# Kernel tuning notes

Hardware: AMD Instinct MI355X
Metric: run time of the kernel (lower is better)

## Reference

```python
import jax, jax.numpy as jnp
import numpy as np

# sizes / constants (mirroring the source module's constants)
M, T_SOL, NX, NY = 12, 64, 256, 256
N_TIMES, NOUT = 50, 256
LX, LY_TARGET = 60.0, 75.0
C_CU_TARGET, C_NI_TARGET = 0.001, 0.0001
T_MAX = 200.0
SIGMA, H, DH = 0.25, 4, 8


def setup_inputs() -> dict:
    key = jax.random.key(0)
    ks = jax.random.split(key, 7)
    u = jax.random.uniform(ks[0], (M, 3), dtype=jnp.float32)
    # rows: (Ly in [30,120], c_Cu in [0,0.0029], c_Ni in [0,0.0018])
    params = jnp.stack([30.0 + 90.0 * u[:, 0], 0.0029 * u[:, 1], 0.0018 * u[:, 2]], axis=1)
    c1_src = jax.random.uniform(ks[1], (M, T_SOL, NX, NY), dtype=jnp.float32) * 0.003
    c2_src = jax.random.uniform(ks[2], (M, T_SOL, NX, NY), dtype=jnp.float32) * 0.002
    Wq = jax.random.normal(ks[3], (H * DH, 3), dtype=jnp.float32) * 0.5
    bq = jax.random.normal(ks[4], (H * DH,), dtype=jnp.float32) * 0.1
    Wk = jax.random.normal(ks[5], (H * DH, 3), dtype=jnp.float32) * 0.5
    bk = jax.random.normal(ks[6], (H * DH,), dtype=jnp.float32) * 0.1
    return {"params": params, "c1_src": c1_src, "c2_src": c2_src,
            "Wq": Wq, "bq": bq, "Wk": Wk, "bk": bk}


def _bilinear_resample(xs, ys, vals, xq, yq):
    """RegularGridInterpolator(linear, fill_value=0) on grid (xs[NX], ys[NY]).
    vals: [T, NX, NY]; query is the outer-product grid xq[PX] x yq[PY].
    Separable bilinear -> [T, PX, PY]."""
    ix = jnp.clip(jnp.searchsorted(xs, xq, side='right') - 1, 0, xs.shape[0] - 2)
    tx = (xq - xs[ix]) / (xs[ix + 1] - xs[ix])
    vx = vals[:, ix, :] * (1.0 - tx)[None, :, None] + vals[:, ix + 1, :] * tx[None, :, None]
    iy = jnp.clip(jnp.searchsorted(ys, yq, side='right') - 1, 0, ys.shape[0] - 2)
    ty = (yq - ys[iy]) / (ys[iy + 1] - ys[iy])
    out = vx[:, :, iy] * (1.0 - ty)[None, None, :] + vx[:, :, iy + 1] * ty[None, None, :]
    inb = ((xq >= xs[0]) & (xq <= xs[-1]))[:, None] & ((yq >= ys[0]) & (yq <= ys[-1]))[None, :]
    return jnp.where(inb[None], out, jnp.float32(0.0))


def _forward(params, c1_src, c2_src, Wq, bq, Wk, bk):
    lys, c_cus, c_nis = params[:, 0], params[:, 1], params[:, 2]
    ly_n = (lys - 30.0) / 90.0
    ccu_n = c_cus / 0.0029
    cni_n = c_nis / 0.0018
    p = jnp.stack([ly_n, ccu_n, cni_n], axis=1)                      # [M,3]
    t = jnp.array([[(LY_TARGET - 30.0) / 90.0,
                    C_CU_TARGET / 0.0029,
                    C_NI_TARGET / 0.0018]], dtype=params.dtype)       # [1,3]
    Q = (t @ Wq.T + bq).reshape(1, H, DH)
    K = (p @ Wk.T + bk).reshape(-1, H, DH)
    attn = jnp.einsum('nhd,mhd->nmh', K, Q) / (DH ** 0.5)            # [M,1,H]
    attn_w = jax.nn.softmax(attn, axis=0).mean(axis=2)[:, 0]         # [M]
    dist2 = (((ly_n - t[0, 0]) / SIGMA) ** 2
             + ((ccu_n - t[0, 1]) / SIGMA) ** 2
             + ((cni_n - t[0, 2]) / SIGMA) ** 2)
    sw = jnp.exp(-dist2 / 2.0)
    sw = sw / sw.sum()
    w = attn_w * sw
    w = w / w.sum()                                                  # [M]

    # grids: source x shared; per-solution y grid rescaled to [0, LY_TARGET]
    xs = jnp.linspace(0.0, LX, NX)
    ys_scaled = (jnp.linspace(0.0, 1.0, NY)[None, :] * lys[:, None]) * (LY_TARGET / lys)[:, None]  # [M,NY]
    xq = jnp.linspace(0.0, LX, NOUT)
    yq = jnp.linspace(0.0, LY_TARGET, NOUT)

    times = jnp.linspace(0.0, min(T_MAX, T_MAX), N_TIMES)
    tidx = jnp.clip((times / T_MAX * T_SOL).astype(jnp.int32), 0, T_SOL - 1)  # [T]
    c1_sel = c1_src[:, tidx]                                          # [M,T,NX,NY]
    c2_sel = c2_src[:, tidx]

    res1, res2 = jax.vmap(
        lambda ys, v1, v2: (_bilinear_resample(xs, ys, v1, xq, yq),
                            _bilinear_resample(xs, ys, v2, xq, yq))
    )(ys_scaled, c1_sel, c2_sel)                                      # each [M,T,NOUT,NOUT]

    c1 = jnp.einsum('m,mtij->tij', w, res1)
    c2 = jnp.einsum('m,mtij->tij', w, res2)
    c1 = c1.at[:, :, 0].set(C_CU_TARGET)
    c2 = c2.at[:, :, -1].set(C_NI_TARGET)
    return jnp.stack([c1, c2])                                        # [2,T,NOUT,NOUT]


def reference(params, c1_src, c2_src, Wq, bq, Wk, bk):
    return _forward(params, c1_src, c2_src, Wq, bq, Wk, bk)
```

## Files before the change

kernel.cpp:

```cpp
#include <hip/hip_runtime.h>

#define MM    12
#define TSOL  64
#define NXX   256
#define NYY   256
#define NTT   50
#define NOUTT 256

__device__ float g_wm1[MM * NOUTT];
__device__ float g_wc [MM * NOUTT];
__device__ float g_wp1[MM * NOUTT];

__global__ __launch_bounds__(256) void ai_setup_kernel(
    const float* __restrict__ params,
    const float* __restrict__ Wq, const float* __restrict__ bq,
    const float* __restrict__ Wk, const float* __restrict__ bk)
{
    const int k = threadIdx.x;
    const int m = blockIdx.x;

    __shared__ float s_attn[MM][4];
    __shared__ float s_sw[MM];
    __shared__ float s_wm;
    __shared__ float s_ys[NYY];

    if (k < MM) {
        float ly = params[k * 3 + 0];
        float p0 = (ly - 30.0f) / 90.0f;
        float p1 = params[k * 3 + 1] / 0.0029f;
        float p2 = params[k * 3 + 2] / 0.0018f;
        const float t0 = 0.5f;
        const float t1 = 0.001f / 0.0029f;
        const float t2 = 0.0001f / 0.0018f;
        for (int h = 0; h < 4; ++h) {
            float acc = 0.0f;
            for (int d = 0; d < 8; ++d) {
                int o = h * 8 + d;
                float q  = t0 * Wq[o * 3 + 0] + t1 * Wq[o * 3 + 1] + t2 * Wq[o * 3 + 2] + bq[o];
                float kv = p0 * Wk[o * 3 + 0] + p1 * Wk[o * 3 + 1] + p2 * Wk[o * 3 + 2] + bk[o];
                acc += kv * q;
            }
            s_attn[k][h] = acc * 0.35355339059327373f;
        }
        float d0 = (p0 - t0) / 0.25f;
        float d1 = (p1 - t1) / 0.25f;
        float d2 = (p2 - t2) / 0.25f;
        s_sw[k] = expf(-(d0 * d0 + d1 * d1 + d2 * d2) * 0.5f);
    }
    __syncthreads();

    if (k == 0) {
        float aw[MM];
        for (int j = 0; j < MM; ++j) aw[j] = 0.0f;
        for (int h = 0; h < 4; ++h) {
            float mx = s_attn[0][h];
            for (int j = 1; j < MM; ++j) mx = fmaxf(mx, s_attn[j][h]);
            float e[MM]; float sum = 0.0f;
            for (int j = 0; j < MM; ++j) { e[j] = expf(s_attn[j][h] - mx); sum += e[j]; }
            for (int j = 0; j < MM; ++j) aw[j] += e[j] / sum;
        }
        float swsum = 0.0f;
        for (int j = 0; j < MM; ++j) swsum += s_sw[j];
        float wj[MM]; float wsum = 0.0f;
        for (int j = 0; j < MM; ++j) {
            wj[j] = (aw[j] * 0.25f) * (s_sw[j] / swsum);
            wsum += wj[j];
        }
        s_wm = wj[m] / wsum;
    }

    {
        float ly  = params[m * 3 + 0];
        float inv = 75.0f / ly;
        float l01 = (float)k * (1.0f / 255.0f);
        s_ys[k] = (l01 * ly) * inv;
    }
    __syncthreads();

    float w  = s_wm;
    float yq = (float)k * (75.0f / 255.0f);
    int l = 0, r = NYY;
    while (l < r) { int mid = (l + r) >> 1; if (s_ys[mid] <= yq) l = mid + 1; else r = mid; }
    int iy = l - 1;
    iy = iy < 0 ? 0 : (iy > NYY - 2 ? NYY - 2 : iy);
    float ty  = (yq - s_ys[iy]) / (s_ys[iy + 1] - s_ys[iy]);
    bool  inb = (yq >= s_ys[0]) && (yq <= s_ys[NYY - 1]);
    float a = inb ? w * (1.0f - ty) : 0.0f;
    float b = inb ? w * ty          : 0.0f;
    bool sel = (iy == k);
    g_wm1[m * NOUTT + k] = sel ? 0.0f : a;
    g_wc [m * NOUTT + k] = sel ? a    : b;
    g_wp1[m * NOUTT + k] = sel ? b    : 0.0f;
}

__global__ __launch_bounds__(256) void ai_resample_kernel(
    const float* __restrict__ c1, const float* __restrict__ c2,
    float* __restrict__ out)
{
    const int tid  = threadIdx.x;
    const int lane = tid & 63;
    const int wv   = tid >> 6;
    const int t    = blockIdx.y;
    const int i    = blockIdx.x * 4 + wv;
    int tsrc = (t * TSOL) / (NTT - 1);
    if (tsrc > TSOL - 1) tsrc = TSOL - 1;
    const int k0 = lane * 4;

    float4 acc1 = {0.f, 0.f, 0.f, 0.f};
    float4 acc2 = {0.f, 0.f, 0.f, 0.f};

#pragma unroll
    for (int m = 0; m < MM; ++m) {
        const float4 wm1 = *(const float4*)&g_wm1[m * NOUTT + k0];
        const float4 wc  = *(const float4*)&g_wc [m * NOUTT + k0];
        const float4 wp1 = *(const float4*)&g_wp1[m * NOUTT + k0];
        const size_t base = ((size_t)(m * TSOL + tsrc) * NXX + (size_t)i) * NYY
                          + (size_t)k0;
        float4 s1 = *(const float4*)(c1 + base);
        float4 s2 = *(const float4*)(c2 + base);

        float l1 = __shfl_up(s1.w, 1);
        float r1 = __shfl_down(s1.x, 1);
        acc1.x += wm1.x * l1   + wc.x * s1.x + wp1.x * s1.y;
        acc1.y += wm1.y * s1.x + wc.y * s1.y + wp1.y * s1.z;
        acc1.z += wm1.z * s1.y + wc.z * s1.z + wp1.z * s1.w;
        acc1.w += wm1.w * s1.z + wc.w * s1.w + wp1.w * r1;

        float l2 = __shfl_up(s2.w, 1);
        float r2 = __shfl_down(s2.x, 1);
        acc2.x += wm1.x * l2   + wc.x * s2.x + wp1.x * s2.y;
        acc2.y += wm1.y * s2.x + wc.y * s2.y + wp1.y * s2.z;
        acc2.z += wm1.z * s2.y + wc.z * s2.z + wp1.z * s2.w;
        acc2.w += wm1.w * s2.z + wc.w * s2.w + wp1.w * r2;
    }

    if (lane == 0)  acc1.x = 0.001f;
    if (lane == 63) acc2.w = 0.0001f;

    *(float4*)&out[((size_t)t * NOUTT + (size_t)i) * NOUTT + (size_t)k0] = acc1;
    *(float4*)&out[((size_t)(NTT + t) * NOUTT + (size_t)i) * NOUTT + (size_t)k0] = acc2;
}

extern "C" void kernel_launch(void* const* d_in, const int* in_sizes, int n_in,
                              void* d_out, int out_size, void* d_ws, size_t ws_size,
                              hipStream_t stream) {
    const float* params = (const float*)d_in[0];
    const float* c1     = (const float*)d_in[1];
    const float* c2     = (const float*)d_in[2];
    const float* Wq     = (const float*)d_in[3];
    const float* bq     = (const float*)d_in[4];
    const float* Wk     = (const float*)d_in[5];
    const float* bk     = (const float*)d_in[6];
    float* out = (float*)d_out;

    ai_setup_kernel<<<dim3(MM), dim3(256), 0, stream>>>(params, Wq, bq, Wk, bk);
    ai_resample_kernel<<<dim3(NOUTT / 4, NTT), dim3(256), 0, stream>>>(c1, c2, out);
}
```

Measured before the change: 403.6 us.

## Stage weight tables in LDS and batch source loads per row

The three weight tables are merged into one contiguous table. Each block copies it into shared memory with direct global-to-LDS loads, so the weights are no longer re-read from global memory for every row. Each block now handles two rows per wave, and the twelve source loads per field are issued together before the FMAs to raise memory-level parallelism. The cost is 36 KB of LDS per block and more registers, which may lower occupancy, and offsets are now computed in 32-bit arithmetic.

```diff
diff --git a/kernel.cpp b/kernel.cpp
--- a/kernel.cpp
+++ b/kernel.cpp
@@ -6,10 +6,9 @@
 #define NYY   256
 #define NTT   50
 #define NOUTT 256
+#define IPB   2
 
-__device__ float g_wm1[MM * NOUTT];
-__device__ float g_wc [MM * NOUTT];
-__device__ float g_wp1[MM * NOUTT];
+__device__ float g_tab3[3 * MM * NOUTT];
 
 __global__ __launch_bounds__(256) void ai_setup_kernel(
     const float* __restrict__ params,
@@ -88,57 +87,86 @@
     float a = inb ? w * (1.0f - ty) : 0.0f;
     float b = inb ? w * ty          : 0.0f;
     bool sel = (iy == k);
-    g_wm1[m * NOUTT + k] = sel ? 0.0f : a;
-    g_wc [m * NOUTT + k] = sel ? a    : b;
-    g_wp1[m * NOUTT + k] = sel ? b    : 0.0f;
+    g_tab3[(0 * MM + m) * NOUTT + k] = sel ? 0.0f : a;
+    g_tab3[(1 * MM + m) * NOUTT + k] = sel ? a    : b;
+    g_tab3[(2 * MM + m) * NOUTT + k] = sel ? b    : 0.0f;
 }
 
 __global__ __launch_bounds__(256) void ai_resample_kernel(
     const float* __restrict__ c1, const float* __restrict__ c2,
     float* __restrict__ out)
 {
+    __shared__ float s_t[3 * MM * NOUTT];
+
     const int tid  = threadIdx.x;
     const int lane = tid & 63;
     const int wv   = tid >> 6;
     const int t    = blockIdx.y;
-    const int i    = blockIdx.x * 4 + wv;
+    const int i0   = blockIdx.x * (4 * IPB);
     int tsrc = (t * TSOL) / (NTT - 1);
     if (tsrc > TSOL - 1) tsrc = TSOL - 1;
     const int k0 = lane * 4;
 
-    float4 acc1 = {0.f, 0.f, 0.f, 0.f};
-    float4 acc2 = {0.f, 0.f, 0.f, 0.f};
+#pragma unroll
+    for (int c = 0; c < 9; ++c) {
+        const float* gp = g_tab3 + c * 1024 + wv * 256 + lane * 4;
+        float*       lp = s_t    + c * 1024 + wv * 256;
+        __builtin_amdgcn_global_load_lds(
+            (const __attribute__((address_space(1))) void*)gp,
+            (__attribute__((address_space(3))) void*)lp, 16, 0, 0);
+    }
+    __syncthreads();
 
 #pragma unroll
-    for (int m = 0; m < MM; ++m) {
-        const float4 wm1 = *(const float4*)&g_wm1[m * NOUTT + k0];
-        const float4 wc  = *(const float4*)&g_wc [m * NOUTT + k0];
-        const float4 wp1 = *(const float4*)&g_wp1[m * NOUTT + k0];
-        const size_t base = ((size_t)(m * TSOL + tsrc) * NXX + (size_t)i) * NYY
-                          + (size_t)k0;
-        float4 s1 = *(const float4*)(c1 + base);
-        float4 s2 = *(const float4*)(c2 + base);
+    for (int r = 0; r < IPB; ++r) {
+        const int i = i0 + r * 4 + wv;
 
-        float l1 = __shfl_up(s1.w, 1);
-        float r1 = __shfl_down(s1.x, 1);
-        acc1.x += wm1.x * l1   + wc.x * s1.x + wp1.x * s1.y;
-        acc1.y += wm1.y * s1.x + wc.y * s1.y + wp1.y * s1.z;
-        acc1.z += wm1.z * s1.y + wc.z * s1.z + wp1.z * s1.w;
-        acc1.w += wm1.w * s1.z + wc.w * s1.w + wp1.w * r1;
+        unsigned int off[MM];
+#pragma unroll
+        for (int m = 0; m < MM; ++m)
+            off[m] = (((unsigned int)(m * TSOL + tsrc) * NXX) + (unsigned int)i) * NYY
+                   + (unsigned int)k0;
 
-        float l2 = __shfl_up(s2.w, 1);
-        float r2 = __shfl_down(s2.x, 1);
-        acc2.x += wm1.x * l2   + wc.x * s2.x + wp1.x * s2.y;
-        acc2.y += wm1.y * s2.x + wc.y * s2.y + wp1.y * s2.z;
-        acc2.z += wm1.z * s2.y + wc.z * s2.z + wp1.z * s2.w;
-        acc2.w += wm1.w * s2.z + wc.w * s2.w + wp1.w * r2;
+        float4 acc1 = {0.f, 0.f, 0.f, 0.f};
+        float4 acc2 = {0.f, 0.f, 0.f, 0.f};
+        float4 st[MM];
+
+#pragma unroll
+        for (int m = 0; m < MM; ++m) st[m] = *(const float4*)(c1 + off[m]);
+#pragma unroll
+        for (int m = 0; m < MM; ++m) {
+            const float4 wm1 = *(const float4*)&s_t[(0 * MM + m) * NOUTT + k0];
+            const float4 wc  = *(const float4*)&s_t[(1 * MM + m) * NOUTT + k0];
+            const float4 wp1 = *(const float4*)&s_t[(2 * MM + m) * NOUTT + k0];
+            float lft = __shfl_up(st[m].w, 1);
+            float rgt = __shfl_down(st[m].x, 1);
+            acc1.x += wm1.x * lft     + wc.x * st[m].x + wp1.x * st[m].y;
+            acc1.y += wm1.y * st[m].x + wc.y * st[m].y + wp1.y * st[m].z;
+            acc1.z += wm1.z * st[m].y + wc.z * st[m].z + wp1.z * st[m].w;
+            acc1.w += wm1.w * st[m].z + wc.w * st[m].w + wp1.w * rgt;
+        }
+
+#pragma unroll
+        for (int m = 0; m < MM; ++m) st[m] = *(const float4*)(c2 + off[m]);
+#pragma unroll
+        for (int m = 0; m < MM; ++m) {
+            const float4 wm1 = *(const float4*)&s_t[(0 * MM + m) * NOUTT + k0];
+            const float4 wc  = *(const float4*)&s_t[(1 * MM + m) * NOUTT + k0];
+            const float4 wp1 = *(const float4*)&s_t[(2 * MM + m) * NOUTT + k0];
+            float lft = __shfl_up(st[m].w, 1);
+            float rgt = __shfl_down(st[m].x, 1);
+            acc2.x += wm1.x * lft     + wc.x * st[m].x + wp1.x * st[m].y;
+            acc2.y += wm1.y * st[m].x + wc.y * st[m].y + wp1.y * st[m].z;
+            acc2.z += wm1.z * st[m].y + wc.z * st[m].z + wp1.z * st[m].w;
+            acc2.w += wm1.w * st[m].z + wc.w * st[m].w + wp1.w * rgt;
+        }
+
+        if (lane == 0)  acc1.x = 0.001f;
+        if (lane == 63) acc2.w = 0.0001f;
+
+        *(float4*)&out[((size_t)t * NOUTT + (size_t)i) * NOUTT + (size_t)k0] = acc1;
+        *(float4*)&out[((size_t)(NTT + t) * NOUTT + (size_t)i) * NOUTT + (size_t)k0] = acc2;
     }
-
-    if (lane == 0)  acc1.x = 0.001f;
-    if (lane == 63) acc2.w = 0.0001f;
-
-    *(float4*)&out[((size_t)t * NOUTT + (size_t)i) * NOUTT + (size_t)k0] = acc1;
-    *(float4*)&out[((size_t)(NTT + t) * NOUTT + (size_t)i) * NOUTT + (size_t)k0] = acc2;
 }
 
 extern "C" void kernel_launch(void* const* d_in, const int* in_sizes, int n_in,
@@ -154,5 +182,5 @@
     float* out = (float*)d_out;
 
     ai_setup_kernel<<<dim3(MM), dim3(256), 0, stream>>>(params, Wq, bq, Wk, bk);
-    ai_resample_kernel<<<dim3(NOUTT / 4, NTT), dim3(256), 0, stream>>>(c1, c2, out);
+    ai_resample_kernel<<<dim3(NOUTT / (4 * IPB), NTT), dim3(256), 0, stream>>>(c1, c2, out);
 }
```

New measurement: 482.1 us. 1.19x slower.

## Compress interpolation weights to one signed coefficient and process several timesteps per block

Applied to the files above, without the earlier changes.

Replaces the three per-column weight arrays with one signed coefficient plus a per-solution scalar weight, loaded once into registers. Each block now loops over five output timesteps, so the coefficient loads are amortized, and it issues all twelve source-row loads before doing any arithmetic to raise memory-level parallelism. The cost is higher register pressure (occupancy hinted at three blocks) and a tenth as many blocks in the grid, which may reduce latency hiding for this bandwidth-bound kernel.

```diff
diff --git a/kernel.cpp b/kernel.cpp
--- a/kernel.cpp
+++ b/kernel.cpp
@@ -6,10 +6,11 @@
 #define NYY   256
 #define NTT   50
 #define NOUTT 256
+#define TPW   5
 
-__device__ float g_wm1[MM * NOUTT];
-__device__ float g_wc [MM * NOUTT];
-__device__ float g_wp1[MM * NOUTT];
+__device__ float g_c[MM * NOUTT];
+__device__ float g_w[MM];
+__device__ float g_w255[MM];
 
 __global__ __launch_bounds__(256) void ai_setup_kernel(
     const float* __restrict__ params,
@@ -88,57 +89,81 @@
     float a = inb ? w * (1.0f - ty) : 0.0f;
     float b = inb ? w * ty          : 0.0f;
     bool sel = (iy == k);
-    g_wm1[m * NOUTT + k] = sel ? 0.0f : a;
-    g_wc [m * NOUTT + k] = sel ? a    : b;
-    g_wp1[m * NOUTT + k] = sel ? b    : 0.0f;
+    g_c[m * NOUTT + k] = sel ? b : -a;
+    if (k == 0)   g_w[m]    = w;
+    if (k == 255) g_w255[m] = inb ? w : 0.0f;
 }
 
-__global__ __launch_bounds__(256) void ai_resample_kernel(
+__global__ __launch_bounds__(256, 3) void ai_resample_kernel(
     const float* __restrict__ c1, const float* __restrict__ c2,
     float* __restrict__ out)
 {
     const int tid  = threadIdx.x;
     const int lane = tid & 63;
     const int wv   = tid >> 6;
-    const int t    = blockIdx.y;
     const int i    = blockIdx.x * 4 + wv;
-    int tsrc = (t * TSOL) / (NTT - 1);
-    if (tsrc > TSOL - 1) tsrc = TSOL - 1;
-    const int k0 = lane * 4;
+    const int tb   = blockIdx.y * TPW;
+    const int k0   = lane * 4;
+    const bool l63 = (lane == 63);
 
-    float4 acc1 = {0.f, 0.f, 0.f, 0.f};
-    float4 acc2 = {0.f, 0.f, 0.f, 0.f};
+    float4 cm[MM];
+#pragma unroll
+    for (int m = 0; m < MM; ++m) cm[m] = *(const float4*)&g_c[m * NOUTT + k0];
+    float wmv[MM], w2v[MM];
+#pragma unroll
+    for (int m = 0; m < MM; ++m) { wmv[m] = g_w[m]; w2v[m] = g_w255[m]; }
+
+#pragma unroll 1
+    for (int j = 0; j < TPW; ++j) {
+        const int t = tb + j;
+        int tsrc = (t * TSOL) / (NTT - 1);
+        if (tsrc > TSOL - 1) tsrc = TSOL - 1;
+        const size_t rowoff = (size_t)tsrc * (NXX * NYY) + (size_t)i * NYY + (size_t)k0;
+
+        float4 acc1 = {0.f, 0.f, 0.f, 0.f};
+        float4 acc2 = {0.f, 0.f, 0.f, 0.f};
+        float4 st[MM];
 
 #pragma unroll
-    for (int m = 0; m < MM; ++m) {
-        const float4 wm1 = *(const float4*)&g_wm1[m * NOUTT + k0];
-        const float4 wc  = *(const float4*)&g_wc [m * NOUTT + k0];
-        const float4 wp1 = *(const float4*)&g_wp1[m * NOUTT + k0];
-        const size_t base = ((size_t)(m * TSOL + tsrc) * NXX + (size_t)i) * NYY
-                          + (size_t)k0;
-        float4 s1 = *(const float4*)(c1 + base);
-        float4 s2 = *(const float4*)(c2 + base);
+        for (int m = 0; m < MM; ++m)
+            st[m] = *(const float4*)(c1 + (size_t)m * (TSOL * NXX * NYY) + rowoff);
+#pragma unroll
+        for (int m = 0; m < MM; ++m) {
+            float4 s = st[m];
+            float lft = __shfl_up(s.w, 1);
+            float rgt = __shfl_down(s.x, 1);
+            float4 c  = cm[m];
+            float wm_ = wmv[m];
+            float w_w = l63 ? w2v[m] : wm_;
+            acc1.x += wm_ * s.x + fabsf(c.x) * (((__float_as_int(c.x) >= 0) ? s.y : lft) - s.x);
+            acc1.y += wm_ * s.y + fabsf(c.y) * (((__float_as_int(c.y) >= 0) ? s.z : s.x) - s.y);
+            acc1.z += wm_ * s.z + fabsf(c.z) * (((__float_as_int(c.z) >= 0) ? s.w : s.y) - s.z);
+            acc1.w += w_w * s.w + fabsf(c.w) * (((__float_as_int(c.w) >= 0) ? rgt : s.z) - s.w);
+        }
 
-        float l1 = __shfl_up(s1.w, 1);
-        float r1 = __shfl_down(s1.x, 1);
-        acc1.x += wm1.x * l1   + wc.x * s1.x + wp1.x * s1.y;
-        acc1.y += wm1.y * s1.x + wc.y * s1.y + wp1.y * s1.z;
-        acc1.z += wm1.z * s1.y + wc.z * s1.z + wp1.z * s1.w;
-        acc1.w += wm1.w * s1.z + wc.w * s1.w + wp1.w * r1;
+#pragma unroll
+        for (int m = 0; m < MM; ++m)
+            st[m] = *(const float4*)(c2 + (size_t)m * (TSOL * NXX * NYY) + rowoff);
+#pragma unroll
+        for (int m = 0; m < MM; ++m) {
+            float4 s = st[m];
+            float lft = __shfl_up(s.w, 1);
+            float rgt = __shfl_down(s.x, 1);
+            float4 c  = cm[m];
+            float wm_ = wmv[m];
+            float w_w = l63 ? w2v[m] : wm_;
+            acc2.x += wm_ * s.x + fabsf(c.x) * (((__float_as_int(c.x) >= 0) ? s.y : lft) - s.x);
+            acc2.y += wm_ * s.y + fabsf(c.y) * (((__float_as_int(c.y) >= 0) ? s.z : s.x) - s.y);
+            acc2.z += wm_ * s.z + fabsf(c.z) * (((__float_as_int(c.z) >= 0) ? s.w : s.y) - s.z);
+            acc2.w += w_w * s.w + fabsf(c.w) * (((__float_as_int(c.w) >= 0) ? rgt : s.z) - s.w);
+        }
 
-        float l2 = __shfl_up(s2.w, 1);
-        float r2 = __shfl_down(s2.x, 1);
-        acc2.x += wm1.x * l2   + wc.x * s2.x + wp1.x * s2.y;
-        acc2.y += wm1.y * s2.x + wc.y * s2.y + wp1.y * s2.z;
-        acc2.z += wm1.z * s2.y + wc.z * s2.z + wp1.z * s2.w;
-        acc2.w += wm1.w * s2.z + wc.w * s2.w + wp1.w * r2;
+        if (lane == 0) acc1.x = 0.001f;
+        if (l63)       acc2.w = 0.0001f;
+
+        *(float4*)&out[((size_t)t * NOUTT + (size_t)i) * NOUTT + (size_t)k0] = acc1;
+        *(float4*)&out[((size_t)(NTT + t) * NOUTT + (size_t)i) * NOUTT + (size_t)k0] = acc2;
     }
-
-    if (lane == 0)  acc1.x = 0.001f;
-    if (lane == 63) acc2.w = 0.0001f;
-
-    *(float4*)&out[((size_t)t * NOUTT + (size_t)i) * NOUTT + (size_t)k0] = acc1;
-    *(float4*)&out[((size_t)(NTT + t) * NOUTT + (size_t)i) * NOUTT + (size_t)k0] = acc2;
 }
 
 extern "C" void kernel_launch(void* const* d_in, const int* in_sizes, int n_in,
@@ -154,5 +179,5 @@
     float* out = (float*)d_out;
 
     ai_setup_kernel<<<dim3(MM), dim3(256), 0, stream>>>(params, Wq, bq, Wk, bk);
-    ai_resample_kernel<<<dim3(NOUTT / 4, NTT), dim3(256), 0, stream>>>(c1, c2, out);
+    ai_resample_kernel<<<dim3(NOUTT / 4, NTT / TPW), dim3(256), 0, stream>>>(c1, c2, out);
 }
```

Measured after the change: 433.4 us. 1.07x slower.
